# Optimization experiments

Measured on AMD Instinct MI355X. Metric: run time of the kernel, lower is better.

## Reference

```python
import jax, jax.numpy as jnp
import numpy as np

GRID_SIZE = 5
SPLINE_ORDER = 3
GRID_LO, GRID_HI = -1.0, 1.0
N_BASIS = GRID_SIZE + SPLINE_ORDER  # 8


def make_grid():
    # Extended knot vector as in efficient-kan: grid_size+2*spline_order+1 points
    h = (GRID_HI - GRID_LO) / GRID_SIZE
    return (jnp.arange(-SPLINE_ORDER, GRID_SIZE + SPLINE_ORDER + 1, dtype=jnp.float32) * h + GRID_LO)  # (12,)


def b_splines(x, grid):
    # Cox-de Boor recursion; x: (...,) -> (..., N_BASIS)
    xg = x[..., None]
    bases = ((xg >= grid[:-1]) & (xg < grid[1:])).astype(x.dtype)
    for k in range(1, SPLINE_ORDER + 1):
        left = (xg - grid[: -(k + 1)]) / (grid[k:-1] - grid[: -(k + 1)]) * bases[..., :-1]
        right = (grid[k + 1:] - xg) / (grid[k + 1:] - grid[1:-k]) * bases[..., 1:]
        bases = left + right
    return bases


def extract_patches3(x):
    # x: (B, C, H, W) -> (B, C, 9, H, W); 3x3 kernel, stride 1, padding 1
    B, C, H, W = x.shape
    xp = jnp.pad(x, ((0, 0), (0, 0), (1, 1), (1, 1)))
    return jnp.stack([xp[:, :, di:di + H, dj:dj + W]
                      for di in range(3) for dj in range(3)], axis=2)


def kan_conv(x, base_w, spline_w, scaler, grid):
    # One KANLinear(9 -> 1) per (out_ch, in_ch) pair, summed over in_ch.
    p = extract_patches3(x)                          # (B, Cin, 9, H, W)
    base = jnp.einsum('biphw,oip->bohw', jax.nn.silu(p), base_w)
    basis = b_splines(p, grid)                       # (B, Cin, 9, H, W, G)
    sw = spline_w * scaler[..., None]                # standalone spline scaler
    spl = jnp.einsum('biphwg,oipg->bohw', basis, sw)
    return base + spl


def maxpool2(x):
    B, C, H, W = x.shape
    return x.reshape(B, C, H // 2, 2, W // 2, 2).max(axis=(3, 5))


def setup_inputs() -> dict:
    key = jax.random.key(0)
    ks = jax.random.split(key, 7)
    return {
        'x': jax.random.normal(ks[0], (2048, 1, 28, 28), dtype=jnp.float32),
        'base_w1': jax.random.normal(ks[1], (2, 1, 9), dtype=jnp.float32) * 0.3,
        'spline_w1': jax.random.normal(ks[2], (2, 1, 9, 8), dtype=jnp.float32) * 0.1,
        'scaler1': jax.random.normal(ks[3], (2, 1, 9), dtype=jnp.float32) * 0.3 + 1.0,
        'base_w2': jax.random.normal(ks[4], (2, 2, 9), dtype=jnp.float32) * 0.3,
        'spline_w2': jax.random.normal(ks[5], (2, 2, 9, 8), dtype=jnp.float32) * 0.1,
        'scaler2': jax.random.normal(ks[6], (2, 2, 9), dtype=jnp.float32) * 0.3 + 1.0,
    }


def reference(x, base_w1, spline_w1, scaler1, base_w2, spline_w2, scaler2):
    grid = make_grid()
    h = maxpool2(kan_conv(x, base_w1, spline_w1, scaler1, grid))   # (B, 2, 14, 14)
    h = maxpool2(kan_conv(h, base_w2, spline_w2, scaler2, grid))   # (B, 2, 7, 7)
    return h.reshape(h.shape[0], -1)                               # (B, 98)
```

## Files before the change

### kernel.cpp

```cpp
#include <hip/hip_runtime.h>
#include <math.h>

typedef _Float16 half_t;
typedef _Float16 h2 __attribute__((ext_vector_type(2)));
typedef unsigned int uint;
typedef unsigned long long u64;

#define TPB 256

__device__ __forceinline__ uint pack_h2f(float a, float b) {
  half_t ha = (half_t)a, hb = (half_t)b;
  unsigned short ua = __builtin_bit_cast(unsigned short, ha);
  unsigned short ub = __builtin_bit_cast(unsigned short, hb);
  return (uint)ua | ((uint)ub << 16);
}

__device__ __forceinline__ float dot8(uint d0, uint d1, uint d2, uint d3,
                                      float sv, const uint* __restrict__ w,
                                      float acc) {
  acc = fmaf(sv, __uint_as_float(w[4]), acc);
#if __has_builtin(__builtin_amdgcn_fdot2)
  acc = __builtin_amdgcn_fdot2(__builtin_bit_cast(h2, d0), __builtin_bit_cast(h2, w[0]), acc, false);
  acc = __builtin_amdgcn_fdot2(__builtin_bit_cast(h2, d1), __builtin_bit_cast(h2, w[1]), acc, false);
  acc = __builtin_amdgcn_fdot2(__builtin_bit_cast(h2, d2), __builtin_bit_cast(h2, w[2]), acc, false);
  acc = __builtin_amdgcn_fdot2(__builtin_bit_cast(h2, d3), __builtin_bit_cast(h2, w[3]), acc, false);
#else
  uint dd[4] = {d0, d1, d2, d3};
#pragma unroll
  for (int k = 0; k < 4; ++k) {
    h2 f = __builtin_bit_cast(h2, dd[k]);
    h2 wv = __builtin_bit_cast(h2, w[k]);
    acc = fmaf((float)f.x, (float)wv.x, acc);
    acc = fmaf((float)f.y, (float)wv.y, acc);
  }
#endif
  return acc;
}

__device__ __forceinline__ void feat_store(float x, uint* __restrict__ slot) {
  float e = __expf(-x);
  float silu = x * __builtin_amdgcn_rcpf(1.0f + e);
  float s = fmaf(x, 2.5f, 5.5f);
  float sf = floorf(s);
  float t = s - sf;
  int p = (int)sf - 3;
  float omt = 1.0f - t, t2 = t * t;
  float B0 = (1.0f / 6.0f) * omt * omt * omt;
  float B3 = (1.0f / 6.0f) * t2 * t;
  float B1 = fmaf(0.5f * t, t2, 2.0f / 3.0f - t2);
  float B2 = 1.0f - B0 - B1 - B3;
  u64 A = ((u64)pack_h2f(B2, B3) << 32) | pack_h2f(B0, B1);
  int n = p < 0 ? -p : 0;
  A = (n >= 4) ? 0ull : (A >> (16 * n));
  int pc = p < 0 ? 0 : (p > 9 ? 9 : p);
  int sh = 16 * pc;
  u64 lo = (sh < 64) ? (A << sh) : 0ull;
  u64 hi = (sh == 0) ? 0ull
         : (sh < 64) ? (A >> (64 - sh))
         : (sh < 128) ? (A << (sh - 64)) : 0ull;
  *(uint2*)slot = make_uint2((uint)lo, (uint)(lo >> 32));
  *(uint2*)(slot + 2) = make_uint2((uint)hi, (uint)(hi >> 32));
  slot[4] = __float_as_uint(silu);
}

__global__ void pack_w(const float* __restrict__ bw1, const float* __restrict__ sw1,
                       const float* __restrict__ sc1, const float* __restrict__ bw2,
                       const float* __restrict__ sw2, const float* __restrict__ sc2,
                       uint* __restrict__ W) {
  const int t = threadIdx.x;
  if (t < 18) {
    const float scv = sc1[t];
    uint* dst = W + t * 5;
#pragma unroll
    for (int j = 0; j < 4; ++j)
      dst[j] = pack_h2f(sw1[t * 8 + 2 * j] * scv, sw1[t * 8 + 2 * j + 1] * scv);
    dst[4] = __float_as_uint(bw1[t]);
  } else if (t < 54) {
    const int q = t - 18;
    const float scv = sc2[q];
    uint* dst = W + 90 + q * 5;
#pragma unroll
    for (int j = 0; j < 4; ++j)
      dst[j] = pack_h2f(sw2[q * 8 + 2 * j] * scv, sw2[q * 8 + 2 * j + 1] * scv);
    dst[4] = __float_as_uint(bw2[q]);
  }
}

__global__ __launch_bounds__(TPB, 5) void kan_fwd(
    const float* __restrict__ x, const uint* __restrict__ W,
    float* __restrict__ out)
{
  __shared__ __align__(16) uint lds[5400 + 2352];
  uint* F1 = lds;
  uint* F2 = lds + 5400;
  float* P = (float*)lds;

  const int tid = threadIdx.x;
  const float* xb = x + (size_t)blockIdx.x * 784;

  for (int ii = tid; ii < 900; ii += TPB) {
    int r = ii / 30, c = ii % 30;
    bool inter = ((uint)(r - 1) < 28u) && ((uint)(c - 1) < 28u);
    int xi = (r - 1) * 28 + (c - 1);
    xi = min(max(xi, 0), 783);
    float xv = xb[xi];
    xv = inter ? xv : 0.0f;
    feat_store(xv, F1 + ii * 6);
  }
  __syncthreads();

  if (tid < 196) {
    const int ph = tid / 14, pw = tid % 14;
    float acc[2][4];
#pragma unroll
    for (int o = 0; o < 2; ++o)
#pragma unroll
      for (int q = 0; q < 4; ++q) acc[o][q] = 0.0f;
#pragma unroll
    for (int r = 0; r < 4; ++r) {
#pragma unroll
      for (int c = 0; c < 4; ++c) {
        const uint* sl = F1 + ((2 * ph + r) * 30 + (2 * pw + c)) * 6;
        uint2 a = *(const uint2*)sl;
        uint2 bq = *(const uint2*)(sl + 2);
        float sv = __uint_as_float(sl[4]);
#pragma unroll
        for (int dh = 0; dh < 2; ++dh) {
          if (r - dh < 0 || r - dh > 2) continue;
#pragma unroll
          for (int dw = 0; dw < 2; ++dw) {
            if (c - dw < 0 || c - dw > 2) continue;
            const int tap = (r - dh) * 3 + (c - dw);
#pragma unroll
            for (int o = 0; o < 2; ++o)
              acc[o][dh * 2 + dw] =
                  dot8(a.x, a.y, bq.x, bq.y, sv, W + (o * 9 + tap) * 5, acc[o][dh * 2 + dw]);
          }
        }
      }
    }
#pragma unroll
    for (int o = 0; o < 2; ++o) {
      float m = fmaxf(fmaxf(acc[o][0], acc[o][1]), fmaxf(acc[o][2], acc[o][3]));
      feat_store(m, F2 + (o * 196 + tid) * 6);
    }
  }
  __syncthreads();

  {
    const int wid = __builtin_amdgcn_readfirstlane(tid >> 6);
    const int lane = tid & 63;
    const uint F0d1 = pack_h2f(1.0f / 48.0f, 23.0f / 48.0f);
    const uint F0d2 = pack_h2f(23.0f / 48.0f, 1.0f / 48.0f);
    if (lane < 49) {
      const int ci = wid & 1;
      const int ph = lane / 7, pw = lane % 7;
      float pa[4] = {0.0f, 0.0f, 0.0f, 0.0f};
#pragma unroll
      for (int r = 0; r < 4; ++r) {
#pragma unroll
        for (int c = 0; c < 4; ++c) {
          int row = 2 * ph + r - 1, col = 2 * pw + c - 1;
          bool ok = ((uint)row < 14u) && ((uint)col < 14u);
          int rcl = min(max(row, 0), 13), ccl = min(max(col, 0), 13);
          const uint* sl = F2 + (ci * 196 + rcl * 14 + ccl) * 6;
          uint2 a = *(const uint2*)sl;
          uint2 bq = *(const uint2*)(sl + 2);
          float sv = ok ? __uint_as_float(sl[4]) : 0.0f;
          uint d0 = ok ? a.x : 0u;
          uint d1 = ok ? a.y : F0d1;
          uint d2 = ok ? bq.x : F0d2;
          uint d3 = ok ? bq.y : 0u;
#pragma unroll
          for (int dh = 0; dh < 2; ++dh) {
            if (r - dh < 0 || r - dh > 2) continue;
#pragma unroll
            for (int dw = 0; dw < 2; ++dw) {
              if (c - dw < 0 || c - dw > 2) continue;
              const int tap = (r - dh) * 3 + (c - dw);
              pa[dh * 2 + dw] =
                  dot8(d0, d1, d2, d3, sv, W + 90 + (wid * 9 + tap) * 5, pa[dh * 2 + dw]);
            }
          }
        }
      }
      *(float4*)&P[(wid * 49 + lane) * 4] = make_float4(pa[0], pa[1], pa[2], pa[3]);
    }
  }
  __syncthreads();

  if (tid < 98) {
    const int o = tid / 49, pos = tid % 49;
    const float4 p0 = *(const float4*)&P[((o * 2 + 0) * 49 + pos) * 4];
    const float4 p1 = *(const float4*)&P[((o * 2 + 1) * 49 + pos) * 4];
    float m = fmaxf(fmaxf(p0.x + p1.x, p0.y + p1.y), fmaxf(p0.z + p1.z, p0.w + p1.w));
    out[(size_t)blockIdx.x * 98 + tid] = m;
  }
}

extern "C" void kernel_launch(void* const* d_in, const int* in_sizes, int n_in,
                              void* d_out, int out_size, void* d_ws, size_t ws_size,
                              hipStream_t stream) {
  const float* x   = (const float*)d_in[0];
  const float* bw1 = (const float*)d_in[1];
  const float* sw1 = (const float*)d_in[2];
  const float* sc1 = (const float*)d_in[3];
  const float* bw2 = (const float*)d_in[4];
  const float* sw2 = (const float*)d_in[5];
  const float* sc2 = (const float*)d_in[6];
  float* out = (float*)d_out;
  uint* W = (uint*)d_ws;
  const int B = in_sizes[0] / 784;
  pack_w<<<1, 64, 0, stream>>>(bw1, sw1, sc1, bw2, sw2, sc2, W);
  kan_fwd<<<B, TPB, 0, stream>>>(x, W, out);
}
```

Measured before the change: 84.71 us.

## Split LDS feature slots into SoA planes with even/odd column deinterleave

Replaces the 6-word array-of-structs feature slot in LDS with three separate planes (low basis pair, high basis pair, silu). Columns are reordered into even and odd halves so the stride-2 accesses of the pooled conv threads hit consecutive addresses. The aim is fewer LDS bank conflicts and a smaller LDS footprint, which may allow more resident blocks. The cost is more complex index arithmetic in every stage.

```diff
diff --git a/kernel.cpp b/kernel.cpp
--- a/kernel.cpp
+++ b/kernel.cpp
@@ -37,7 +37,9 @@
   return acc;
 }
 
-__device__ __forceinline__ void feat_store(float x, uint* __restrict__ slot) {
+__device__ __forceinline__ void feat_store(float x, uint* __restrict__ A,
+                                           uint* __restrict__ Bq,
+                                           uint* __restrict__ S) {
   float e = __expf(-x);
   float silu = x * __builtin_amdgcn_rcpf(1.0f + e);
   float s = fmaf(x, 2.5f, 5.5f);
@@ -49,18 +51,18 @@
   float B3 = (1.0f / 6.0f) * t2 * t;
   float B1 = fmaf(0.5f * t, t2, 2.0f / 3.0f - t2);
   float B2 = 1.0f - B0 - B1 - B3;
-  u64 A = ((u64)pack_h2f(B2, B3) << 32) | pack_h2f(B0, B1);
+  u64 Av = ((u64)pack_h2f(B2, B3) << 32) | pack_h2f(B0, B1);
   int n = p < 0 ? -p : 0;
-  A = (n >= 4) ? 0ull : (A >> (16 * n));
+  Av = (n >= 4) ? 0ull : (Av >> (16 * n));
   int pc = p < 0 ? 0 : (p > 9 ? 9 : p);
   int sh = 16 * pc;
-  u64 lo = (sh < 64) ? (A << sh) : 0ull;
+  u64 lo = (sh < 64) ? (Av << sh) : 0ull;
   u64 hi = (sh == 0) ? 0ull
-         : (sh < 64) ? (A >> (64 - sh))
-         : (sh < 128) ? (A << (sh - 64)) : 0ull;
-  *(uint2*)slot = make_uint2((uint)lo, (uint)(lo >> 32));
-  *(uint2*)(slot + 2) = make_uint2((uint)hi, (uint)(hi >> 32));
-  slot[4] = __float_as_uint(silu);
+         : (sh < 64) ? (Av >> (64 - sh))
+         : (sh < 128) ? (Av << (sh - 64)) : 0ull;
+  *(uint2*)A = make_uint2((uint)lo, (uint)(lo >> 32));
+  *(uint2*)Bq = make_uint2((uint)hi, (uint)(hi >> 32));
+  *S = __float_as_uint(silu);
 }
 
 __global__ void pack_w(const float* __restrict__ bw1, const float* __restrict__ sw1,
@@ -90,22 +92,30 @@
     const float* __restrict__ x, const uint* __restrict__ W,
     float* __restrict__ out)
 {
-  __shared__ __align__(16) uint lds[5400 + 2352];
-  uint* F1 = lds;
-  uint* F2 = lds + 5400;
+  __shared__ __align__(16) uint lds[6460];
+  uint* F1A = lds;
+  uint* F1B = lds + 1800;
+  uint* F1S = lds + 3600;
+  uint* F2A = lds + 4500;
+  uint* F2B = lds + 5284;
+  uint* F2S = lds + 6068;
   float* P = (float*)lds;
 
   const int tid = threadIdx.x;
   const float* xb = x + (size_t)blockIdx.x * 784;
 
   for (int ii = tid; ii < 900; ii += TPB) {
-    int r = ii / 30, c = ii % 30;
+    int hp = ii >= 450 ? 1 : 0;
+    int k = ii - hp * 450;
+    int r = k / 15, cc = k % 15;
+    int c = 2 * cc + hp;
     bool inter = ((uint)(r - 1) < 28u) && ((uint)(c - 1) < 28u);
     int xi = (r - 1) * 28 + (c - 1);
     xi = min(max(xi, 0), 783);
     float xv = xb[xi];
     xv = inter ? xv : 0.0f;
-    feat_store(xv, F1 + ii * 6);
+    int sidx = r * 30 + cc + hp * 15;
+    feat_store(xv, F1A + sidx * 2, F1B + sidx * 2, F1S + sidx);
   }
   __syncthreads();
 
@@ -120,10 +130,10 @@
     for (int r = 0; r < 4; ++r) {
 #pragma unroll
       for (int c = 0; c < 4; ++c) {
-        const uint* sl = F1 + ((2 * ph + r) * 30 + (2 * pw + c)) * 6;
-        uint2 a = *(const uint2*)sl;
-        uint2 bq = *(const uint2*)(sl + 2);
-        float sv = __uint_as_float(sl[4]);
+        const int sidx = (2 * ph + r) * 30 + (pw + (c >> 1)) + (c & 1) * 15;
+        uint2 a = *(const uint2*)(F1A + sidx * 2);
+        uint2 bq = *(const uint2*)(F1B + sidx * 2);
+        float sv = __uint_as_float(F1S[sidx]);
 #pragma unroll
         for (int dh = 0; dh < 2; ++dh) {
           if (r - dh < 0 || r - dh > 2) continue;
@@ -142,7 +152,8 @@
 #pragma unroll
     for (int o = 0; o < 2; ++o) {
       float m = fmaxf(fmaxf(acc[o][0], acc[o][1]), fmaxf(acc[o][2], acc[o][3]));
-      feat_store(m, F2 + (o * 196 + tid) * 6);
+      int fidx = o * 196 + ph * 14 + (pw >> 1) + (pw & 1) * 7;
+      feat_store(m, F2A + fidx * 2, F2B + fidx * 2, F2S + fidx);
     }
   }
   __syncthreads();
@@ -163,10 +174,10 @@
           int row = 2 * ph + r - 1, col = 2 * pw + c - 1;
           bool ok = ((uint)row < 14u) && ((uint)col < 14u);
           int rcl = min(max(row, 0), 13), ccl = min(max(col, 0), 13);
-          const uint* sl = F2 + (ci * 196 + rcl * 14 + ccl) * 6;
-          uint2 a = *(const uint2*)sl;
-          uint2 bq = *(const uint2*)(sl + 2);
-          float sv = ok ? __uint_as_float(sl[4]) : 0.0f;
+          const int fidx = ci * 196 + rcl * 14 + (ccl >> 1) + (ccl & 1) * 7;
+          uint2 a = *(const uint2*)(F2A + fidx * 2);
+          uint2 bq = *(const uint2*)(F2B + fidx * 2);
+          float sv = ok ? __uint_as_float(F2S[fidx]) : 0.0f;
           uint d0 = ok ? a.x : 0u;
           uint d1 = ok ? a.y : F0d1;
           uint d2 = ok ? bq.x : F0d2;
```

Result: slower. 86.46 us (+2.1%).
